# Kernel optimization log

Hardware: AMD Instinct MI355X
Metric: run time of the kernel (lower is better)

The kernel has to match this reference:

```python
import jax, jax.numpy as jnp
import numpy as np

B, T, V, D, H, DENSE, C = 512, 300, 50000, 128, 256, 256, 14


def setup_inputs() -> dict:
    key = jax.random.key(0)
    ks = jax.random.split(key, 12)
    inputs_arrays = jax.random.randint(ks[0], (B, T), 0, V + 1)
    traj_lens = jax.random.randint(ks[1], (B,), 1, T)
    emb = jax.random.normal(ks[2], (V + 1, D), jnp.float32) * 0.02
    emb = emb.at[0].set(0.0)  # padding_idx=0
    # torch.nn.LSTMCell parameters, gate order i,f,g,o along dim 0 (4H)
    W_ih = jax.random.normal(ks[3], (4 * H, D), jnp.float32) * (1.0 / np.sqrt(D))
    W_hh = jax.random.normal(ks[4], (4 * H, H), jnp.float32) * (1.0 / np.sqrt(H))
    b_ih = jnp.zeros((4 * H,), jnp.float32)
    # keras-style forget-gate bias = 1 (second chunk)
    b_hh = jnp.concatenate([jnp.zeros((H,)), jnp.ones((H,)), jnp.zeros((2 * H,))]).astype(jnp.float32)
    W3 = jax.random.normal(ks[5], (DENSE, H * T), jnp.float32) * (1.0 / np.sqrt(H * T))
    b3 = jnp.zeros((DENSE,), jnp.float32)
    W4 = jax.random.normal(ks[6], (C, DENSE), jnp.float32) * (1.0 / np.sqrt(DENSE))
    b4 = jnp.zeros((C,), jnp.float32)
    return {"inputs_arrays": inputs_arrays, "traj_lens": traj_lens,
            "emb": emb, "W_ih": W_ih, "W_hh": W_hh, "b_ih": b_ih, "b_hh": b_hh,
            "W3": W3, "b3": b3, "W4": W4, "b4": b4}


def _lstm_forward(x, W_hh, b_hh, gx):
    # gx: [T, B, 4H] precomputed input-side gates; scan the recurrence
    Hn = W_hh.shape[1]

    def step(carry, gx_t):
        h, c = carry
        gates = gx_t + h @ W_hh.T + b_hh  # [B, 4H]
        i, f, g, o = jnp.split(gates, 4, axis=-1)
        i, f, o = jax.nn.sigmoid(i), jax.nn.sigmoid(f), jax.nn.sigmoid(o)
        g = jnp.tanh(g)
        c = f * c + i * g
        h = o * jnp.tanh(c)
        return (h, c), h

    Bn = gx.shape[1]
    init = (jnp.zeros((Bn, Hn), gx.dtype), jnp.zeros((Bn, Hn), gx.dtype))
    _, hs = jax.lax.scan(step, init, gx)  # hs: [T, B, H]
    return hs


def reference(inputs_arrays, traj_lens, emb, W_ih, W_hh, b_ih, b_hh, W3, b3, W4, b4):
    x = emb[inputs_arrays]                                   # [B, T, D]
    gx = jnp.einsum('btd,gd->tbg', x, W_ih) + b_ih           # [T, B, 4H]
    hs = _lstm_forward(x, W_hh, b_hh, gx)                    # [T, B, H]
    outputs = jnp.transpose(hs, (1, 0, 2))                   # [B, T, H]
    last_out = outputs.reshape(outputs.shape[0], -1)         # [B, T*H]
    dens_out = jax.nn.relu(last_out @ W3.T + b3)             # [B, 256]
    return jax.nn.softmax(dens_out @ W4.T + b4, axis=1)      # [B, C]
```

## Files before the change

kernel.cpp:

```cpp
#include <hip/hip_runtime.h>

#define BB    512
#define TT    300
#define DD    128
#define HH    256
#define GG    1024
#define DNS   256
#define NC    14
#define KDIM  76800

typedef _Float16 f16;
typedef _Float16 f16x8 __attribute__((ext_vector_type(8)));
typedef float    f32x4 __attribute__((ext_vector_type(4)));

__device__ __forceinline__ float sigf(float x){ return 1.0f / (1.0f + __expf(-x)); }
__device__ __forceinline__ float tanhfast(float x){ return 2.0f / (1.0f + __expf(-2.0f*x)) - 1.0f; }

__global__ void k_gather(const int* __restrict__ idx, const float* __restrict__ emb,
                         f16* __restrict__ xbuf)
{
    int gid = blockIdx.x * 256 + threadIdx.x;
    if (gid >= BB*TT*DD/4) return;
    int bt = gid >> 5;
    int c4 = gid & 31;
    int v  = idx[bt];
    const float4 e = *(const float4*)(emb + (size_t)v*DD + c4*4);
    union { f16 h[4]; uint2 u; } o;
    o.h[0]=(f16)e.x; o.h[1]=(f16)e.y; o.h[2]=(f16)e.z; o.h[3]=(f16)e.w;
    *(uint2*)(xbuf + (size_t)bt*DD + c4*4) = o.u;
}

__global__ __launch_bounds__(512) void k_lstm(
    const f16* __restrict__ xbuf, f16* __restrict__ hs,
    const float* __restrict__ Wih, const float* __restrict__ Whh,
    const float* __restrict__ bih, const float* __restrict__ bhh,
    unsigned int* hpp)
{
    __shared__ f16   Ast[16*392];
    __shared__ float gbuf[16*260];
    __shared__ float biasS[256];

    const int tid  = threadIdx.x;
    const int bsI  = blockIdx.x & 63;
    const int sI   = blockIdx.x >> 6;
    const int r0   = bsI*8, j0 = sI*64;
    const int wv   = tid >> 6, lane = tid & 63;
    const int q16  = lane & 15, quad = lane >> 4;

    f16x8 bf[2][12];
    #pragma unroll
    for (int nt = 0; nt < 2; ++nt) {
        const int ql   = (wv*2 + nt)*16 + q16;
        const int drow = ql >> 2, ty = ql & 3;
        const int Grow = ty*HH + j0 + drow;
        const float* wh = Whh + (size_t)Grow*HH;
        #pragma unroll
        for (int kk = 0; kk < 8; ++kk) {
            const float* p = wh + kk*32 + quad*8;
            float4 f0 = *(const float4*)p, f1 = *(const float4*)(p+4);
            f16x8 b;
            b[0]=(f16)f0.x; b[1]=(f16)f0.y; b[2]=(f16)f0.z; b[3]=(f16)f0.w;
            b[4]=(f16)f1.x; b[5]=(f16)f1.y; b[6]=(f16)f1.z; b[7]=(f16)f1.w;
            bf[nt][kk] = b;
        }
        const float* wi = Wih + (size_t)Grow*DD;
        #pragma unroll
        for (int kk = 0; kk < 4; ++kk) {
            const float* p = wi + kk*32 + quad*8;
            float4 f0 = *(const float4*)p, f1 = *(const float4*)(p+4);
            f16x8 b;
            b[0]=(f16)f0.x; b[1]=(f16)f0.y; b[2]=(f16)f0.z; b[3]=(f16)f0.w;
            b[4]=(f16)f1.x; b[5]=(f16)f1.y; b[6]=(f16)f1.z; b[7]=(f16)f1.w;
            bf[nt][8+kk] = b;
        }
    }
    if (tid < 256) {
        const int drow = tid >> 2, ty = tid & 3;
        const int Grow = ty*HH + j0 + drow;
        biasS[tid] = bih[Grow] + bhh[Grow];
    }

    float c = 0.0f;
    const int f0 = lane*3;
    const int d0 = (f0   < j0) ? f0   : f0+64;
    const int d1 = (f0+1 < j0) ? f0+1 : f0+1+64;
    const int d2 = (f0+2 < j0) ? f0+2 : f0+2+64;

    for (int t = 0; t < TT; ++t) {
        if (tid < 128) {
            int row = tid >> 4, ch = tid & 15;
            uint4 val = *(const uint4*)(xbuf + ((size_t)(r0+row)*TT + t)*DD + ch*8);
            *(uint4*)(Ast + (size_t)row*392 + 256 + ch*8) = val;
        }
        if (t > 0) {
            unsigned int* pb = hpp + (size_t)((t-1)&1)*BB*HH + (size_t)(r0+wv)*HH;
            const unsigned int tgt = (unsigned)(t-1);
            unsigned int v0, v1, v2;
            for (;;) {
                v0 = __hip_atomic_load(pb+d0, __ATOMIC_RELAXED, __HIP_MEMORY_SCOPE_AGENT);
                v1 = __hip_atomic_load(pb+d1, __ATOMIC_RELAXED, __HIP_MEMORY_SCOPE_AGENT);
                v2 = __hip_atomic_load(pb+d2, __ATOMIC_RELAXED, __HIP_MEMORY_SCOPE_AGENT);
                if (((v0>>16)==tgt) & ((v1>>16)==tgt) & ((v2>>16)==tgt)) break;
                __builtin_amdgcn_s_sleep(1);
            }
            union { unsigned short us; f16 hf; } u0, u1, u2;
            u0.us = (unsigned short)v0; u1.us = (unsigned short)v1; u2.us = (unsigned short)v2;
            Ast[wv*392 + d0] = u0.hf;
            Ast[wv*392 + d1] = u1.hf;
            Ast[wv*392 + d2] = u2.hf;
        } else {
            Ast[wv*392 + d0] = (f16)0.f;
            Ast[wv*392 + d1] = (f16)0.f;
            Ast[wv*392 + d2] = (f16)0.f;
            Ast[wv*392 + j0 + lane] = (f16)0.f;
        }
        __syncthreads();

        f32x4 acc0 = {0.f,0.f,0.f,0.f}, acc1 = {0.f,0.f,0.f,0.f};
        const f16* arow = Ast + q16*392 + quad*8;
        #pragma unroll
        for (int kk = 0; kk < 12; ++kk) {
            f16x8 a = *(const f16x8*)(arow + kk*32);
            acc0 = __builtin_amdgcn_mfma_f32_16x16x32_f16(a, bf[0][kk], acc0, 0, 0, 0);
            acc1 = __builtin_amdgcn_mfma_f32_16x16x32_f16(a, bf[1][kk], acc1, 0, 0, 0);
        }
        #pragma unroll
        for (int r = 0; r < 4; ++r) {
            gbuf[(quad*4+r)*260 + (wv*2+0)*16 + q16] = acc0[r];
            gbuf[(quad*4+r)*260 + (wv*2+1)*16 + q16] = acc1[r];
        }
        __syncthreads();

        float h;
        {
            const float4 g = *(const float4*)(gbuf + wv*260 + lane*4);
            const float4 bs = *(const float4*)(biasS + lane*4);
            float gi = g.x + bs.x;
            float gf = g.y + bs.y;
            float gg = g.z + bs.z;
            float go = g.w + bs.w;
            float iv = sigf(gi), fv = sigf(gf), gv = tanhfast(gg), ov = sigf(go);
            c = fv*c + iv*gv;
            h = ov * tanhfast(c);
        }
        union { unsigned short us; f16 hf; } cv; cv.hf = (f16)h;
        __hip_atomic_store(hpp + (size_t)(t&1)*BB*HH + (size_t)(r0+wv)*HH + j0 + lane,
                           ((unsigned)t << 16) | cv.us,
                           __ATOMIC_RELAXED, __HIP_MEMORY_SCOPE_AGENT);
        Ast[wv*392 + j0 + lane] = cv.hf;
        hs[((size_t)(r0+wv)*TT + t)*HH + j0 + lane] = cv.hf;
    }
}

__global__ __launch_bounds__(256) void k_dense(
    const f16* __restrict__ hs, const float* __restrict__ W3, float* __restrict__ part)
{
    __shared__ f16 Ap[128*40];
    __shared__ f16 Bp[128*40];
    const int tid = threadIdx.x;
    const int kb = blockIdx.x & 31, tn = (blockIdx.x >> 5) & 1, tm = blockIdx.x >> 6;
    const int m0 = tm*128, n0 = tn*128;
    const long k0 = (long)kb * 2400;
    const int wv = tid >> 6, lane = tid & 63, q16 = lane & 15, quad = lane >> 4;

    f32x4 acc[2][8];
    #pragma unroll
    for (int a = 0; a < 2; ++a)
        #pragma unroll
        for (int b = 0; b < 8; ++b) acc[a][b] = (f32x4){0.f,0.f,0.f,0.f};

    for (int ks = 0; ks < 75; ++ks) {
        const long kbase = k0 + ks*32;
        #pragma unroll
        for (int rep = 0; rep < 4; ++rep) {
            int cid = tid + rep*256;
            int rrow = (cid & 511) >> 2;
            int c4   = cid & 3;
            if (cid < 512) {
                const f16* src = hs + (size_t)(m0+rrow)*KDIM + kbase + c4*8;
                *(uint4*)(Ap + rrow*40 + c4*8) = *(const uint4*)src;
            } else {
                const float* src = W3 + (size_t)(n0+rrow)*KDIM + kbase + c4*8;
                float4 f0 = *(const float4*)src, f1 = *(const float4*)(src+4);
                union { f16 h[8]; uint4 u; } o;
                o.h[0]=(f16)f0.x; o.h[1]=(f16)f0.y; o.h[2]=(f16)f0.z; o.h[3]=(f16)f0.w;
                o.h[4]=(f16)f1.x; o.h[5]=(f16)f1.y; o.h[6]=(f16)f1.z; o.h[7]=(f16)f1.w;
                *(uint4*)(Bp + rrow*40 + c4*8) = o.u;
            }
        }
        __syncthreads();

        f16x8 a0 = *(const f16x8*)(Ap + ((wv*2+0)*16 + q16)*40 + quad*8);
        f16x8 a1 = *(const f16x8*)(Ap + ((wv*2+1)*16 + q16)*40 + quad*8);
        #pragma unroll
        for (int ns = 0; ns < 8; ++ns) {
            f16x8 b = *(const f16x8*)(Bp + (ns*16 + q16)*40 + quad*8);
            acc[0][ns] = __builtin_amdgcn_mfma_f32_16x16x32_f16(a0, b, acc[0][ns], 0,0,0);
            acc[1][ns] = __builtin_amdgcn_mfma_f32_16x16x32_f16(a1, b, acc[1][ns], 0,0,0);
        }
        __syncthreads();
    }
    #pragma unroll
    for (int ms = 0; ms < 2; ++ms)
        #pragma unroll
        for (int ns = 0; ns < 8; ++ns)
            #pragma unroll
            for (int r = 0; r < 4; ++r) {
                int m = m0 + (wv*2+ms)*16 + quad*4 + r;
                int n = n0 + ns*16 + q16;
                part[(size_t)kb*BB*DNS + (size_t)m*DNS + n] = acc[ms][ns][r];
            }
}

__global__ void k_reduce(const float* __restrict__ part, const float* __restrict__ b3,
                         float* __restrict__ dens)
{
    int g = blockIdx.x * 256 + threadIdx.x;
    if (g >= BB*DNS) return;
    int n = g & 255;
    float s = b3[n];
    #pragma unroll
    for (int kb = 0; kb < 32; ++kb) s += part[(size_t)kb*BB*DNS + g];
    dens[g] = fmaxf(s, 0.0f);
}

__global__ __launch_bounds__(64) void k_final(
    const float* __restrict__ dens, const float* __restrict__ W4,
    const float* __restrict__ b4, float* __restrict__ out)
{
    const int b = blockIdx.x, lane = threadIdx.x;
    const float4 dv = *(const float4*)(dens + (size_t)b*DNS + lane*4);
    float lg[NC];
    #pragma unroll
    for (int cc = 0; cc < NC; ++cc) {
        const float4 w = *(const float4*)(W4 + (size_t)cc*DNS + lane*4);
        float v = dv.x*w.x + dv.y*w.y + dv.z*w.z + dv.w*w.w;
        #pragma unroll
        for (int off = 32; off; off >>= 1) v += __shfl_xor(v, off, 64);
        lg[cc] = v + b4[cc];
    }
    if (lane == 0) {
        float m = lg[0];
        #pragma unroll
        for (int cc = 1; cc < NC; ++cc) m = fmaxf(m, lg[cc]);
        float e[NC], s = 0.f;
        #pragma unroll
        for (int cc = 0; cc < NC; ++cc) { e[cc] = __expf(lg[cc]-m); s += e[cc]; }
        const float inv = 1.0f/s;
        #pragma unroll
        for (int cc = 0; cc < NC; ++cc) out[(size_t)b*NC + cc] = e[cc]*inv;
    }
}

extern "C" void kernel_launch(void* const* d_in, const int* in_sizes, int n_in,
                              void* d_out, int out_size, void* d_ws, size_t ws_size,
                              hipStream_t stream)
{
    const int*   idx = (const int*)  d_in[0];
    const float* emb = (const float*)d_in[2];
    const float* Wih = (const float*)d_in[3];
    const float* Whh = (const float*)d_in[4];
    const float* bih = (const float*)d_in[5];
    const float* bhh = (const float*)d_in[6];
    const float* W3  = (const float*)d_in[7];
    const float* b3  = (const float*)d_in[8];
    const float* W4  = (const float*)d_in[9];
    const float* b4  = (const float*)d_in[10];
    float* out = (float*)d_out;

    char* ws = (char*)d_ws;
    f16*   xbuf = (f16*)  (ws);
    f16*   hs   = (f16*)  (ws + 39321600);
    float* part = (float*)(ws + 117964800);
    float* dens = (float*)(ws + 134742016);
    unsigned int* hpp = (unsigned int*)part;

    k_gather<<<19200, 256, 0, stream>>>(idx, emb, xbuf);
    k_lstm  <<<256, 512, 0, stream>>>(xbuf, hs, Wih, Whh, bih, bhh, hpp);
    k_dense <<<256, 256, 0, stream>>>(hs, W3, part);
    k_reduce<<<512, 256, 0, stream>>>(part, b3, dens);
    k_final <<<BB, 64, 0, stream>>>(dens, W4, b4, out);
}
```

Baseline: 948.4 us.

## Split LSTM hidden dim across two blocks and ping-pong two row groups

The recurrent kernel now splits the hidden dimension across two cooperating blocks of 128 units each instead of four of 64, halving the grid. Each block processes its 8 rows as two interleaved groups of 4, so the cross-block wait for one group's partner data overlaps with compute on the other group. The partner's value is prefetched speculatively, and each thread polls only one word instead of three. Per-block weight registers double (bf[4][12]), which risks register pressure and spills, and MFMA rows are half-used (only 4 of 16 A rows carry real batch rows).

```diff
diff --git a/kernel.cpp b/kernel.cpp
--- a/kernel.cpp
+++ b/kernel.cpp
@@ -37,22 +37,23 @@
     unsigned int* hpp)
 {
     __shared__ f16   Ast[16*392];
-    __shared__ float gbuf[16*260];
-    __shared__ float biasS[256];
+    __shared__ float gbuf[4*520];
+    __shared__ float biasS[512];
 
     const int tid  = threadIdx.x;
     const int bsI  = blockIdx.x & 63;
     const int sI   = blockIdx.x >> 6;
-    const int r0   = bsI*8, j0 = sI*64;
+    const int r0   = bsI*8;
+    const int j0   = sI*128, fj0 = 128 - j0;
     const int wv   = tid >> 6, lane = tid & 63;
     const int q16  = lane & 15, quad = lane >> 4;
 
-    f16x8 bf[2][12];
-    #pragma unroll
-    for (int nt = 0; nt < 2; ++nt) {
-        const int ql   = (wv*2 + nt)*16 + q16;
-        const int drow = ql >> 2, ty = ql & 3;
-        const int Grow = ty*HH + j0 + drow;
+    f16x8 bf[4][12];
+    #pragma unroll
+    for (int nt = 0; nt < 4; ++nt) {
+        const int ql   = (wv*4 + nt)*16 + q16;
+        const int dl   = ql >> 2, ty = ql & 3;
+        const int Grow = ty*HH + j0 + dl;
         const float* wh = Whh + (size_t)Grow*HH;
         #pragma unroll
         for (int kk = 0; kk < 8; ++kk) {
@@ -74,81 +75,95 @@
             bf[nt][8+kk] = b;
         }
     }
-    if (tid < 256) {
-        const int drow = tid >> 2, ty = tid & 3;
-        const int Grow = ty*HH + j0 + drow;
-        biasS[tid] = bih[Grow] + bhh[Grow];
-    }
-
-    float c = 0.0f;
-    const int f0 = lane*3;
-    const int d0 = (f0   < j0) ? f0   : f0+64;
-    const int d1 = (f0+1 < j0) ? f0+1 : f0+1+64;
-    const int d2 = (f0+2 < j0) ? f0+2 : f0+2+64;
+    {
+        const int dl = tid >> 2, ty = tid & 3;
+        biasS[tid] = bih[ty*HH + j0 + dl] + bhh[ty*HH + j0 + dl];
+    }
+    for (int i = tid; i < 16*392*2/8; i += 512)
+        ((unsigned long long*)Ast)[i] = 0ull;
+    __syncthreads();
+
+    float          cst[2]  = {0.f, 0.f};
+    unsigned short hReg[2] = {0, 0};
+    const int prow = tid >> 7;
+    const int d    = tid & 127;
+    unsigned int pref = 0;
 
     for (int t = 0; t < TT; ++t) {
-        if (tid < 128) {
-            int row = tid >> 4, ch = tid & 15;
-            uint4 val = *(const uint4*)(xbuf + ((size_t)(r0+row)*TT + t)*DD + ch*8);
-            *(uint4*)(Ast + (size_t)row*392 + 256 + ch*8) = val;
-        }
-        if (t > 0) {
-            unsigned int* pb = hpp + (size_t)((t-1)&1)*BB*HH + (size_t)(r0+wv)*HH;
-            const unsigned int tgt = (unsigned)(t-1);
-            unsigned int v0, v1, v2;
-            for (;;) {
-                v0 = __hip_atomic_load(pb+d0, __ATOMIC_RELAXED, __HIP_MEMORY_SCOPE_AGENT);
-                v1 = __hip_atomic_load(pb+d1, __ATOMIC_RELAXED, __HIP_MEMORY_SCOPE_AGENT);
-                v2 = __hip_atomic_load(pb+d2, __ATOMIC_RELAXED, __HIP_MEMORY_SCOPE_AGENT);
-                if (((v0>>16)==tgt) & ((v1>>16)==tgt) & ((v2>>16)==tgt)) break;
-                __builtin_amdgcn_s_sleep(1);
-            }
-            union { unsigned short us; f16 hf; } u0, u1, u2;
-            u0.us = (unsigned short)v0; u1.us = (unsigned short)v1; u2.us = (unsigned short)v2;
-            Ast[wv*392 + d0] = u0.hf;
-            Ast[wv*392 + d1] = u1.hf;
-            Ast[wv*392 + d2] = u2.hf;
-        } else {
-            Ast[wv*392 + d0] = (f16)0.f;
-            Ast[wv*392 + d1] = (f16)0.f;
-            Ast[wv*392 + d2] = (f16)0.f;
-            Ast[wv*392 + j0 + lane] = (f16)0.f;
-        }
-        __syncthreads();
-
-        f32x4 acc0 = {0.f,0.f,0.f,0.f}, acc1 = {0.f,0.f,0.f,0.f};
-        const f16* arow = Ast + q16*392 + quad*8;
-        #pragma unroll
-        for (int kk = 0; kk < 12; ++kk) {
-            f16x8 a = *(const f16x8*)(arow + kk*32);
-            acc0 = __builtin_amdgcn_mfma_f32_16x16x32_f16(a, bf[0][kk], acc0, 0, 0, 0);
-            acc1 = __builtin_amdgcn_mfma_f32_16x16x32_f16(a, bf[1][kk], acc1, 0, 0, 0);
-        }
-        #pragma unroll
-        for (int r = 0; r < 4; ++r) {
-            gbuf[(quad*4+r)*260 + (wv*2+0)*16 + q16] = acc0[r];
-            gbuf[(quad*4+r)*260 + (wv*2+1)*16 + q16] = acc1[r];
-        }
-        __syncthreads();
-
-        float h;
-        {
-            const float4 g = *(const float4*)(gbuf + wv*260 + lane*4);
-            const float4 bs = *(const float4*)(biasS + lane*4);
-            float gi = g.x + bs.x;
-            float gf = g.y + bs.y;
-            float gg = g.z + bs.z;
-            float go = g.w + bs.w;
-            float iv = sigf(gi), fv = sigf(gf), gv = tanhfast(gg), ov = sigf(go);
-            c = fv*c + iv*gv;
-            h = ov * tanhfast(c);
-        }
-        union { unsigned short us; f16 hf; } cv; cv.hf = (f16)h;
-        __hip_atomic_store(hpp + (size_t)(t&1)*BB*HH + (size_t)(r0+wv)*HH + j0 + lane,
-                           ((unsigned)t << 16) | cv.us,
-                           __ATOMIC_RELAXED, __HIP_MEMORY_SCOPE_AGENT);
-        Ast[wv*392 + j0 + lane] = cv.hf;
-        hs[((size_t)(r0+wv)*TT + t)*HH + j0 + lane] = cv.hf;
+        #pragma unroll
+        for (int p = 0; p < 2; ++p) {
+            const int rb = r0 + p*4;
+            if (tid < 64) {
+                int row = tid >> 4, ch = tid & 15;
+                *(uint4*)(Ast + (size_t)row*392 + 256 + ch*8) =
+                    *(const uint4*)(xbuf + ((size_t)(rb+row)*TT + t)*DD + ch*8);
+            }
+            if (t > 0) {
+                union { unsigned short us; f16 hf; } uo; uo.us = hReg[p];
+                Ast[prow*392 + j0 + d] = uo.hf;
+                const unsigned tgt = (unsigned)(t-1);
+                unsigned w = pref;
+                unsigned int* ap = hpp + (size_t)((t-1)&1)*BB*HH
+                                       + (size_t)(rb+prow)*HH + fj0 + d;
+                while ((w >> 16) != tgt) {
+                    __builtin_amdgcn_s_sleep(1);
+                    w = __hip_atomic_load(ap, __ATOMIC_RELAXED,
+                                          __HIP_MEMORY_SCOPE_AGENT);
+                }
+                union { unsigned short us; f16 hf; } uf; uf.us = (unsigned short)w;
+                Ast[prow*392 + fj0 + d] = uf.hf;
+            } else {
+                Ast[prow*392 + j0 + d]  = (f16)0.f;
+                Ast[prow*392 + fj0 + d] = (f16)0.f;
+            }
+            __syncthreads();
+
+            f32x4 acc[4];
+            #pragma unroll
+            for (int nt = 0; nt < 4; ++nt) acc[nt] = (f32x4){0.f,0.f,0.f,0.f};
+            const f16* arow = Ast + q16*392 + quad*8;
+            #pragma unroll
+            for (int kk = 0; kk < 12; ++kk) {
+                f16x8 a = *(const f16x8*)(arow + kk*32);
+                #pragma unroll
+                for (int nt = 0; nt < 4; ++nt)
+                    acc[nt] = __builtin_amdgcn_mfma_f32_16x16x32_f16(a, bf[nt][kk],
+                                                                     acc[nt], 0, 0, 0);
+            }
+            if (quad == 0) {
+                #pragma unroll
+                for (int nt = 0; nt < 4; ++nt)
+                    #pragma unroll
+                    for (int r = 0; r < 4; ++r)
+                        gbuf[r*520 + (wv*4+nt)*16 + q16] = acc[nt][r];
+            }
+            __syncthreads();
+
+            float h;
+            {
+                const float4 g  = *(const float4*)(gbuf  + prow*520 + d*4);
+                const float4 bs = *(const float4*)(biasS + d*4);
+                float gi = g.x + bs.x, gf = g.y + bs.y;
+                float gg = g.z + bs.z, go = g.w + bs.w;
+                float iv = sigf(gi), fv = sigf(gf), gv = tanhfast(gg), ov = sigf(go);
+                float c = fv*cst[p] + iv*gv;
+                cst[p] = c;
+                h = ov * tanhfast(c);
+            }
+            union { unsigned short us; f16 hf; } cv; cv.hf = (f16)h;
+            hReg[p] = cv.us;
+            __hip_atomic_store(hpp + (size_t)(t&1)*BB*HH + (size_t)(rb+prow)*HH + j0 + d,
+                               ((unsigned)t << 16) | cv.us,
+                               __ATOMIC_RELAXED, __HIP_MEMORY_SCOPE_AGENT);
+            hs[((size_t)(rb+prow)*TT + t)*HH + j0 + d] = cv.hf;
+            {
+                const int tn = (p == 0) ? t : t + 1;
+                unsigned int* apn = hpp + (size_t)((tn-1)&1)*BB*HH
+                                        + (size_t)(r0 + (1-p)*4 + prow)*HH + fj0 + d;
+                pref = __hip_atomic_load(apn, __ATOMIC_RELAXED,
+                                         __HIP_MEMORY_SCOPE_AGENT);
+            }
+        }
     }
 }
 
@@ -276,7 +291,7 @@
     unsigned int* hpp = (unsigned int*)part;
 
     k_gather<<<19200, 256, 0, stream>>>(idx, emb, xbuf);
-    k_lstm  <<<256, 512, 0, stream>>>(xbuf, hs, Wih, Whh, bih, bhh, hpp);
+    k_lstm  <<<128, 512, 0, stream>>>(xbuf, hs, Wih, Whh, bih, bhh, hpp);
     k_dense <<<256, 256, 0, stream>>>(hs, W3, part);
     k_reduce<<<512, 256, 0, stream>>>(part, b3, dens);
     k_final <<<BB, 64, 0, stream>>>(dens, W4, b4, out);
```

After: 1.911 ms. 2.01x slower.
